# Performance work log

Measured on AMD Instinct MI355X. Metric: run time of the kernel, lower is better.

## Reference

```python
import jax, jax.numpy as jnp
import numpy as np

N = 8192
IN_F = 512
OUT_F = 64
ALPHA = 0.2        # LeakyReLU slope
L_ITERS = 3        # RobustSum iterations
EPS = 0.01
GAMMA = 4.0
T = 1.0
NEG_BIG = -9e15


def setup_inputs() -> dict:
    key = jax.random.key(0)
    k1, k2, k3, k4 = jax.random.split(key, 4)
    x = jax.random.normal(k1, (N, IN_F), dtype=jnp.float32)
    adj = jax.random.randint(k2, (N, N), 0, 2, dtype=jnp.int32)
    # xavier-uniform-like init scales
    limW = 1.414 * np.sqrt(6.0 / (IN_F + OUT_F))
    W = jax.random.uniform(k3, (IN_F, OUT_F), dtype=jnp.float32, minval=-limW, maxval=limW)
    lima = 1.414 * np.sqrt(6.0 / (2 * OUT_F + 1))
    a = jax.random.uniform(k4, (2 * OUT_F, 1), dtype=jnp.float32, minval=-lima, maxval=lima)
    return {"adj": adj, "input": x, "W": W, "a": a}


def _robust_sum_mcp(A, V):
    # M = A @ V, then IRLS-style reweighted aggregation (norm='MCP')
    M = A @ V
    for _ in range(L_ITERS):
        Md = jax.lax.stop_gradient(M)
        Vd = jax.lax.stop_gradient(V)
        # pairwise Euclidean distance [N, N] (fused form of torch.cdist)
        d2 = (jnp.sum(Md * Md, axis=1, keepdims=True)
              + jnp.sum(Vd * Vd, axis=1)[None, :]
              - 2.0 * (Md @ Vd.T))
        dist = jnp.sqrt(jnp.maximum(d2, 0.0))
        w = 1.0 / (dist + EPS) - 1.0 / GAMMA
        w = jnp.maximum(w, EPS)          # w[w < eps] = eps
        ww = w * A
        denom = jnp.maximum(jnp.sum(jnp.abs(ww), axis=-1, keepdims=True), 1e-12)
        ww_norm = ww / denom             # F.normalize(p=1, dim=-1)
        M = (1.0 - T) * M + T * (ww_norm @ V)
    return M


def reference(adj, input, W, a):
    adj_f = adj.astype(jnp.float32)
    h = input @ W                                     # [N, OUT_F]
    a1 = a[:OUT_F, 0]                                 # [OUT_F]
    a2 = a[OUT_F:, 0]                                 # [OUT_F]
    # fused equivalent of cat([h_i, h_j]) @ a : e_ij = lrelu(h_i.a1 + h_j.a2)
    e = jax.nn.leaky_relu((h @ a1)[:, None] + (h @ a2)[None, :], ALPHA)  # [N, N]
    scores = adj_f * e + (1.0 - adj_f) * NEG_BIG
    attention = jax.nn.softmax(scores, axis=1)
    # dropout omitted (eval mode / dropout=0.0)
    h_prime = _robust_sum_mcp(attention, h)
    return jax.nn.elu(h_prime)                        # concat=True
```

## Files before the change

kernel.cpp:

```cpp
#include <hip/hip_runtime.h>
#include <hip/hip_bf16.h>

typedef __attribute__((ext_vector_type(8))) short s8v;
typedef __attribute__((ext_vector_type(4))) short s4v;
typedef __attribute__((ext_vector_type(4))) float f4v;

static __device__ __forceinline__ short f2bf(float f){
  unsigned int u = __float_as_uint(f);
  u = (u + 0x7FFFu + ((u >> 16) & 1u)) >> 16;
  return (short)u;
}

static __device__ __forceinline__ s4v pack4(float a, float b, float c, float d){
  union { s4v v; __hip_bfloat162 h[2]; } u;
  u.h[0] = __float22bfloat162_rn(make_float2(a, b));
  u.h[1] = __float22bfloat162_rn(make_float2(c, d));
  return u.v;
}

static __device__ __forceinline__ f4v mfma16(s4v a, s4v b, f4v c){
  return __builtin_amdgcn_mfma_f32_16x16x16bf16_1k(a, b, c, 0, 0, 0);
}

__global__ __launch_bounds__(256) void k_h(const float* __restrict__ x,
                                           const float* __restrict__ W,
                                           float* __restrict__ h){
  int wid = threadIdx.x >> 6, lane = threadIdx.x & 63;
  int r0 = (blockIdx.x * 4 + wid) * 8;
  const float* xr = x + (size_t)r0 * 512;
  float acc[8] = {0.f,0.f,0.f,0.f,0.f,0.f,0.f,0.f};
  #pragma unroll 4
  for (int k = 0; k < 512; ++k){
    float wv = W[k*64 + lane];
    #pragma unroll
    for (int r = 0; r < 8; ++r)
      acc[r] = fmaf(xr[(size_t)r*512 + k], wv, acc[r]);
  }
  #pragma unroll
  for (int r = 0; r < 8; ++r)
    h[(size_t)(r0 + r)*64 + lane] = acc[r];
}

__global__ __launch_bounds__(256) void k_prep(const float* __restrict__ h,
                                              const float* __restrict__ a,
                                              short* __restrict__ VbfSw,
                                              short* __restrict__ VTsw,
                                              float* __restrict__ F,
                                              float2* __restrict__ EG,
                                              float* __restrict__ V2arr,
                                              float* __restrict__ Pv2,
                                              float* __restrict__ Pv2x,
                                              float* __restrict__ Pg,
                                              float* __restrict__ Vpart){
  __shared__ float t[64][65];
  const int tid = threadIdx.x;
  const int lane = tid & 63, w = tid >> 6;
  const int lo = lane & 15, hi = lane >> 4;
  const int i0 = blockIdx.x * 64;
  #pragma unroll
  for (int it = 0; it < 16; ++it){
    int r = w * 16 + it;
    t[r][lane] = h[(size_t)(i0 + r) * 64 + lane];
  }
  __syncthreads();
  #pragma unroll
  for (int ks = 0; ks < 2; ++ks){
    s8v o;
    #pragma unroll
    for (int e = 0; e < 8; ++e)
      o[e] = f2bf(t[w*16 + lo][ks*32 + hi*8 + e]);
    *(s8v*)(VbfSw + ((size_t)(i0/16 + w)*2 + ks)*512 + lane*8) = o;
  }
  const int p = w >> 1;
  #pragma unroll
  for (int oo = 0; oo < 2; ++oo){
    const int ot = (w & 1) * 2 + oo;
    s8v o;
    #pragma unroll
    for (int e = 0; e < 8; ++e){
      int parity = e >> 2, q = e & 3;
      o[e] = f2bf(t[(p*2 + parity)*16 + hi*4 + q][ot*16 + lo]);
    }
    *(s8v*)(VTsw + ((size_t)(i0/32 + p)*4 + ot)*512 + lane*8) = o;
  }
  if (tid < 64){
    const int r = tid;
    float f = 0.f, g = 0.f, v2 = 0.f;
    #pragma unroll 8
    for (int o = 0; o < 64; ++o){
      float hv = t[r][o];
      f  = fmaf(hv, a[o],      f);
      g  = fmaf(hv, a[64 + o], g);
      v2 = fmaf(hv, hv,        v2);
    }
    const int row = i0 + r;
    F[row] = f;
    V2arr[row] = v2;
    EG[row] = make_float2(__expf(g), __expf(0.2f * g));
    float vmin = v2, vmax = v2, gmx = g;
    #pragma unroll
    for (int off = 32; off; off >>= 1){
      vmin = fminf(vmin, __shfl_xor(vmin, off));
      vmax = fmaxf(vmax, __shfl_xor(vmax, off));
      gmx  = fmaxf(gmx,  __shfl_xor(gmx,  off));
    }
    if (r == 0){ Pv2[blockIdx.x] = vmin; Pv2x[blockIdx.x] = vmax; Pg[blockIdx.x] = gmx; }
    float cs = 0.f;
    #pragma unroll 8
    for (int rr = 0; rr < 64; ++rr) cs += t[rr][tid];
    Vpart[(size_t)blockIdx.x * 64 + tid] = cs;
  }
}

__global__ __launch_bounds__(512, 4) void k_fused(
    const int* __restrict__ adj,
    const float2* __restrict__ EG, const float* __restrict__ V2arr,
    const float* __restrict__ F,
    const float* __restrict__ Pv2, const float* __restrict__ Pv2x,
    const float* __restrict__ Pg,
    const float* __restrict__ Vpart,
    const short* __restrict__ VbfSw, const short* __restrict__ VTsw,
    unsigned long long* __restrict__ adjbits,
    float* __restrict__ out)
{
  __shared__ float numT[8][64][16];
  __shared__ float denL[8][16];
  __shared__ float Mlds[16][68];
  __shared__ float M1L[16][68];
  __shared__ __align__(16) short Mb16[16][64];
  __shared__ float CiL[16], rm2L[16], uaiL[16];
  __shared__ float VmeanL[64];
  __shared__ float TminS[128], TmaxS[128];
  __shared__ float gmaxS, v2minS, rmnS, rmxS;
  __shared__ int actL, chgL, emptyL;

  const int tid  = threadIdx.x;
  const int w    = tid >> 6;
  const int lane = tid & 63;
  const int lo = lane & 15, hi = lane >> 4;
  const int r0 = blockIdx.x << 4;
  const int i  = r0 + lo;

  if (tid < 64){
    float v = fminf(Pv2[tid], Pv2[tid + 64]);
    float g = fmaxf(Pg[tid],  Pg[tid + 64]);
    #pragma unroll
    for (int off = 32; off; off >>= 1){
      v = fminf(v, __shfl_xor(v, off));
      g = fmaxf(g, __shfl_xor(g, off));
    }
    if (tid == 0){ v2minS = v; gmaxS = g; actL = 0; emptyL = 0; }
  }
  if (tid >= 64 && tid < 192){
    const int b = tid - 64;
    TminS[b] = sqrtf(Pv2[b]);
    TmaxS[b] = sqrtf(Pv2x[b]);
  }
  __syncthreads();

  const float fi   = F[i];
  const float gmax = gmaxS;
  const float z    = fi + gmax;
  const float B    = fmaxf(z, 0.2f * z);
  const float e1s  = __expf(fi - B);
  const float e2s  = __expf(0.2f * fi - B);

  const int* arow = adj + (size_t)i * 8192 + hi*4;

  const f4v zero4 = {0.f,0.f,0.f,0.f};
  f4v pacc[4] = {zero4, zero4, zero4, zero4};
  float pden = 0.f;

  for (int c = w; c < 128; c += 8){
    const int* ap = arow + (c << 6);
    s4v wwpk[4];
    unsigned long long mrow = 0ull;
    #pragma unroll
    for (int nt = 0; nt < 4; ++nt){
      const int jb = (c << 6) + nt*16 + hi*4;
      const int4 av4 = *(const int4*)(ap + nt*16);
      const int ab[4] = {av4.x, av4.y, av4.z, av4.w};
      const f4v u0 = *(const f4v*)(EG + jb);
      const f4v u1 = *(const f4v*)(EG + jb + 2);
      const float ega[4] = {u0[0], u0[2], u1[0], u1[2]};
      const float egb[4] = {u0[1], u0[3], u1[1], u1[3]};
      float wwv[4];
      #pragma unroll
      for (int q = 0; q < 4; ++q){
        float u = fmaxf(e1s * ega[q], e2s * egb[q]);
        u = ab[q] ? u : 0.f;
        pden += u;
        wwv[q] = u;
      }
      const unsigned nib = (unsigned)ab[0] | ((unsigned)ab[1] << 1)
                         | ((unsigned)ab[2] << 2) | ((unsigned)ab[3] << 3);
      mrow |= (unsigned long long)nib << (nt*16 + hi*4);
      wwpk[nt] = pack4(wwv[0], wwv[1], wwv[2], wwv[3]);
    }
    mrow |= __shfl_xor(mrow, 16);
    mrow |= __shfl_xor(mrow, 32);
    if (hi == 0) adjbits[(size_t)c * 8192 + i] = mrow;

    const short* vt = VTsw + (size_t)c*4096 + lane*8;
    #pragma unroll
    for (int p = 0; p < 2; ++p){
      #pragma unroll
      for (int ot = 0; ot < 4; ++ot){
        s8v v8 = *(const s8v*)(vt + (p*4 + ot)*512);
        s4v aLo = {v8[0], v8[1], v8[2], v8[3]};
        s4v aHi = {v8[4], v8[5], v8[6], v8[7]};
        pacc[ot] = mfma16(aLo, wwpk[2*p],   pacc[ot]);
        pacc[ot] = mfma16(aHi, wwpk[2*p+1], pacc[ot]);
      }
    }
  }

  pden += __shfl_xor(pden, 16);
  pden += __shfl_xor(pden, 32);
  if (lane < 16) denL[w][lane] = pden;
  #pragma unroll
  for (int ot = 0; ot < 4; ++ot)
    #pragma unroll
    for (int q = 0; q < 4; ++q)
      numT[w][ot*16 + hi*4 + q][lo] = pacc[ot][q];
  __syncthreads();

  {
    const int ii = tid & 15;
    const int o  = tid >> 4;
    float den = 0.f;
    #pragma unroll
    for (int w2 = 0; w2 < 8; ++w2) den += denL[w2][ii];
    if (o == 0){
      uaiL[ii] = (den <= 0.f) ? (1.0f / 8192.0f) : 0.f;
      if (den <= 0.f) emptyL = 1;
    }
    den = fmaxf(den, 1e-30f);
    const float rden = 1.0f / den;
    #pragma unroll
    for (int rep = 0; rep < 2; ++rep){
      const int oo = o + rep*32;
      float num = 0.f;
      #pragma unroll
      for (int w2 = 0; w2 < 8; ++w2) num += numT[w2][oo][ii];
      Mlds[ii][oo] = num * rden;
    }
    if (tid < 16){
      float fb = F[r0 + tid];
      float zb = fb + gmax;
      float Bb = fmaxf(zb, 0.2f * zb);
      CiL[tid] = Bb + __logf(den);
    }
  }
  __syncthreads();

  if (emptyL){
    if (tid < 64){
      float s = 0.f;
      for (int b = 0; b < 128; ++b) s += Vpart[(size_t)b*64 + tid];
      VmeanL[tid] = s * (1.0f / 8192.0f);
    }
    __syncthreads();
    {
      const int r = tid >> 5, c2 = (tid & 31) << 1;
      if (uaiL[r] > 0.f){ Mlds[r][c2] = VmeanL[c2]; Mlds[r][c2+1] = VmeanL[c2+1]; }
    }
    __syncthreads();
  }

  if (tid < 16){
    float s2 = 0.f;
    #pragma unroll 8
    for (int o = 0; o < 64; ++o) s2 = fmaf(Mlds[tid][o], Mlds[tid][o], s2);
    rm2L[tid] = s2;
    if (sqrtf(s2) > sqrtf(v2minS) - 3.85f) actL = 1;
    float mn = s2, mx = s2;
    #pragma unroll
    for (int off = 8; off; off >>= 1){
      mn = fminf(mn, __shfl_xor(mn, off));
      mx = fmaxf(mx, __shfl_xor(mx, off));
    }
    if (tid == 0){ rmnS = sqrtf(mn); rmxS = sqrtf(mx); }
  }
  __syncthreads();

  if (actL){
    {
      const int r = tid >> 5, c2 = (tid & 31) << 1;
      float a0 = Mlds[r][c2], a1 = Mlds[r][c2+1];
      M1L[r][c2] = a0;  M1L[r][c2+1] = a1;
      Mb16[r][c2] = f2bf(a0); Mb16[r][c2+1] = f2bf(a1);
    }
    const float e1c = __expf(fi - CiL[lo]);
    const float e2c = __expf(0.2f * fi - CiL[lo]);
    const float uai = uaiL[lo];
    __syncthreads();

    for (int pass = 0; pass < 3; ++pass){
      if (tid == 0) chgL = 0;
      __syncthreads();
      const float rm2 = rm2L[lo];
      const float gHi = rmxS + 4.35f;
      const float gLo = rmnS - 4.35f;
      s8v bM[2];
      #pragma unroll
      for (int ks = 0; ks < 2; ++ks)
        bM[ks] = *(const s8v*)&Mb16[lo][ks*32 + hi*8];

      f4v cacc[4] = {zero4, zero4, zero4, zero4};
      float cden = 0.f;

      for (int c = w; c < 128; c += 8){
        if (TminS[c] > gHi || TmaxS[c] < gLo) continue;
        f4v acc[4] = {zero4, zero4, zero4, zero4};
        const short* vb = VbfSw + (size_t)c*4096 + lane*8;
        #pragma unroll
        for (int nt = 0; nt < 4; ++nt){
          #pragma unroll
          for (int ks = 0; ks < 2; ++ks){
            s8v av = *(const s8v*)(vb + (nt*2 + ks)*512);
            acc[nt] = __builtin_amdgcn_mfma_f32_16x16x32_bf16(av, bM[ks], acc[nt], 0, 0, 0);
          }
        }
        f4v d2s[4];
        float dmin = 1e30f;
        #pragma unroll
        for (int nt = 0; nt < 4; ++nt){
          const int jb = (c << 6) + nt*16 + hi*4;
          const f4v v2q = *(const f4v*)(V2arr + jb);
          #pragma unroll
          for (int q = 0; q < 4; ++q){
            float d2 = fmaf(-2.0f, acc[nt][q], rm2 + v2q[q]);
            d2s[nt][q] = d2;
            dmin = fminf(dmin, d2);
          }
        }
        if (__any(dmin < 14.75f)){
          const unsigned long long mrow = adjbits[(size_t)c * 8192 + i];
          s4v wwpk[4];
          #pragma unroll
          for (int nt = 0; nt < 4; ++nt){
            const int jb = (c << 6) + nt*16 + hi*4;
            const unsigned nib = (unsigned)(mrow >> (nt*16 + hi*4)) & 0xFu;
            const f4v u0 = *(const f4v*)(EG + jb);
            const f4v u1 = *(const f4v*)(EG + jb + 2);
            const float ega[4] = {u0[0], u0[2], u1[0], u1[2]};
            const float egb[4] = {u0[1], u0[3], u1[1], u1[3]};
            float wwv[4];
            #pragma unroll
            for (int q = 0; q < 4; ++q){
              float A = fmaxf(e1c * ega[q], e2c * egb[q]);
              A = ((nib >> q) & 1u) ? A : uai;
              float dist  = sqrtf(fmaxf(d2s[nt][q], 0.f));
              float delta = fmaxf(__builtin_amdgcn_rcpf(dist + 0.01f) - 0.26f, 0.f);
              float ww = delta * A;
              cden += ww;
              wwv[q] = ww;
            }
            wwpk[nt] = pack4(wwv[0], wwv[1], wwv[2], wwv[3]);
          }
          const short* vt = VTsw + (size_t)c*4096 + lane*8;
          #pragma unroll
          for (int p = 0; p < 2; ++p){
            #pragma unroll
            for (int ot = 0; ot < 4; ++ot){
              s8v v8 = *(const s8v*)(vt + (p*4 + ot)*512);
              s4v aLo = {v8[0], v8[1], v8[2], v8[3]};
              s4v aHi = {v8[4], v8[5], v8[6], v8[7]};
              cacc[ot] = mfma16(aLo, wwpk[2*p],   cacc[ot]);
              cacc[ot] = mfma16(aHi, wwpk[2*p+1], cacc[ot]);
            }
          }
        }
      }

      if (__any(cden > 0.f)) chgL = 1;
      __syncthreads();
      if (!chgL) break;
      {
        float cd = cden;
        cd += __shfl_xor(cd, 16);
        cd += __shfl_xor(cd, 32);
        if (lane < 16) denL[w][lane] = cd;
        #pragma unroll
        for (int ot = 0; ot < 4; ++ot)
          #pragma unroll
          for (int q = 0; q < 4; ++q)
            numT[w][ot*16 + hi*4 + q][lo] = cacc[ot][q];
        __syncthreads();
        {
          const int ii = tid & 15;
          const int o  = tid >> 4;
          float den = 0.f;
          #pragma unroll
          for (int w2 = 0; w2 < 8; ++w2) den += denL[w2][ii];
          const float rden = 1.0f / (0.01f + den);
          #pragma unroll
          for (int rep = 0; rep < 2; ++rep){
            const int oo = o + rep*32;
            float num = 0.f;
            #pragma unroll
            for (int w2 = 0; w2 < 8; ++w2) num += numT[w2][oo][ii];
            Mlds[ii][oo] = fmaf(0.01f, M1L[ii][oo], num) * rden;
          }
        }
        __syncthreads();
        {
          const int r = tid >> 5, c2 = (tid & 31) << 1;
          Mb16[r][c2]   = f2bf(Mlds[r][c2]);
          Mb16[r][c2+1] = f2bf(Mlds[r][c2+1]);
        }
        if (tid < 16){
          float s2 = 0.f;
          #pragma unroll 8
          for (int o = 0; o < 64; ++o) s2 = fmaf(Mlds[tid][o], Mlds[tid][o], s2);
          rm2L[tid] = s2;
          float mn = s2, mx = s2;
          #pragma unroll
          for (int off = 8; off; off >>= 1){
            mn = fminf(mn, __shfl_xor(mn, off));
            mx = fmaxf(mx, __shfl_xor(mx, off));
          }
          if (tid == 0){ rmnS = sqrtf(mn); rmxS = sqrtf(mx); }
        }
        __syncthreads();
      }
    }
  }
  __syncthreads();

  #pragma unroll
  for (int rr = 0; rr < 2; ++rr){
    const int ir = w*2 + rr;
    const float v = Mlds[ir][lane];
    out[(size_t)(r0 + ir) * 64 + lane] = (v > 0.f) ? v : (__expf(v) - 1.0f);
  }
}

extern "C" void kernel_launch(void* const* d_in, const int* in_sizes, int n_in,
                              void* d_out, int out_size, void* d_ws, size_t ws_size,
                              hipStream_t stream){
  (void)in_sizes; (void)n_in; (void)out_size; (void)ws_size;
  const int*   adj = (const int*)d_in[0];
  const float* x   = (const float*)d_in[1];
  const float* W   = (const float*)d_in[2];
  const float* a   = (const float*)d_in[3];
  float* out = (float*)d_out;
  char* ws = (char*)d_ws;

  float* h     = (float*)(ws);
  short* VbfSw = (short*)(ws + (2u << 20));
  short* VTsw  = (short*)(ws + (3u << 20));
  float* F     = (float*)(ws + (4u << 20));
  float* V2arr = (float*)(ws + (4u << 20) + (32u << 10));
  float2* EG   = (float2*)(ws + (4u << 20) + (64u << 10));
  float* Vpart = (float*)(ws + (4u << 20) + (128u << 10));
  float* Pv2   = (float*)(ws + (4u << 20) + (160u << 10));
  float* Pg    = (float*)(ws + (4u << 20) + (161u << 10));
  float* Pv2x  = (float*)(ws + (4u << 20) + (162u << 10));
  unsigned long long* adjbits = (unsigned long long*)(ws + (5u << 20));

  k_h    <<<256, 256, 0, stream>>>(x, W, h);
  k_prep <<<128, 256, 0, stream>>>(h, a, VbfSw, VTsw, F, EG, V2arr, Pv2, Pv2x, Pg, Vpart);
  k_fused<<<512, 512, 0, stream>>>(adj, EG, V2arr, F, Pv2, Pv2x, Pg, Vpart, VbfSw, VTsw, adjbits, out);
}
```

Measured before the change: 142.8 us.

## Skip stale far column tiles in IRLS passes, prefetch adj, retile input projection

Three changes. The input projection kernel now handles 4 rows per wave instead of 8, reads x as float4 and launches twice as many blocks. The first adjacency sweep prefetches the next chunk's adjacency ints into registers while working on the current chunk. In the reweighting passes, each wave records the minimum row-to-column distance per tile and, across passes, adds a bound on how far the M rows have moved; a tile is skipped when that stale minimum still exceeds the cutoff. This saves distance-MFMA work in later passes at the cost of extra reductions, shared-memory atomics and a barrier per pass, and it relies on the distance bound being conservative enough to keep results correct.

```diff
diff --git a/kernel.cpp b/kernel.cpp
--- a/kernel.cpp
+++ b/kernel.cpp
@@ -26,18 +26,23 @@
                                            const float* __restrict__ W,
                                            float* __restrict__ h){
   int wid = threadIdx.x >> 6, lane = threadIdx.x & 63;
-  int r0 = (blockIdx.x * 4 + wid) * 8;
+  int r0 = (blockIdx.x * 4 + wid) * 4;
   const float* xr = x + (size_t)r0 * 512;
-  float acc[8] = {0.f,0.f,0.f,0.f,0.f,0.f,0.f,0.f};
-  #pragma unroll 4
-  for (int k = 0; k < 512; ++k){
-    float wv = W[k*64 + lane];
-    #pragma unroll
-    for (int r = 0; r < 8; ++r)
-      acc[r] = fmaf(xr[(size_t)r*512 + k], wv, acc[r]);
+  float acc[4] = {0.f,0.f,0.f,0.f};
+  #pragma unroll 2
+  for (int k = 0; k < 512; k += 4){
+    const float w0 = W[(k+0)*64 + lane];
+    const float w1 = W[(k+1)*64 + lane];
+    const float w2 = W[(k+2)*64 + lane];
+    const float w3 = W[(k+3)*64 + lane];
+    #pragma unroll
+    for (int r = 0; r < 4; ++r){
+      const float4 xv = *(const float4*)(xr + (size_t)r*512 + k);
+      acc[r] = fmaf(xv.x, w0, fmaf(xv.y, w1, fmaf(xv.z, w2, fmaf(xv.w, w3, acc[r]))));
+    }
   }
   #pragma unroll
-  for (int r = 0; r < 8; ++r)
+  for (int r = 0; r < 4; ++r)
     h[(size_t)(r0 + r)*64 + lane] = acc[r];
 }
 
@@ -131,6 +136,9 @@
   __shared__ float CiL[16], rm2L[16], uaiL[16];
   __shared__ float VmeanL[64];
   __shared__ float TminS[128], TmaxS[128];
+  __shared__ float aminS[8][16], staleS[8][16];
+  __shared__ float d2rowS[16];
+  __shared__ float dMaxS;
   __shared__ float gmaxS, v2minS, rmnS, rmxS;
   __shared__ int actL, chgL, emptyL;
 
@@ -171,15 +179,26 @@
   f4v pacc[4] = {zero4, zero4, zero4, zero4};
   float pden = 0.f;
 
+  int4 curA[4];
+  {
+    const int* ap0 = arow + (w << 6);
+    #pragma unroll
+    for (int nt = 0; nt < 4; ++nt) curA[nt] = *(const int4*)(ap0 + nt*16);
+  }
   for (int c = w; c < 128; c += 8){
-    const int* ap = arow + (c << 6);
+    const int cn = c + 8;
+    int4 nxtA[4];
+    if (cn < 128){
+      const int* ap2 = arow + (cn << 6);
+      #pragma unroll
+      for (int nt = 0; nt < 4; ++nt) nxtA[nt] = *(const int4*)(ap2 + nt*16);
+    }
     s4v wwpk[4];
     unsigned long long mrow = 0ull;
     #pragma unroll
     for (int nt = 0; nt < 4; ++nt){
       const int jb = (c << 6) + nt*16 + hi*4;
-      const int4 av4 = *(const int4*)(ap + nt*16);
-      const int ab[4] = {av4.x, av4.y, av4.z, av4.w};
+      const int ab[4] = {curA[nt].x, curA[nt].y, curA[nt].z, curA[nt].w};
       const f4v u0 = *(const f4v*)(EG + jb);
       const f4v u1 = *(const f4v*)(EG + jb + 2);
       const float ega[4] = {u0[0], u0[2], u1[0], u1[2]};
@@ -213,6 +232,10 @@
         pacc[ot] = mfma16(aHi, wwpk[2*p+1], pacc[ot]);
       }
     }
+    if (cn < 128){
+      #pragma unroll
+      for (int nt = 0; nt < 4; ++nt) curA[nt] = nxtA[nt];
+    }
   }
 
   pden += __shfl_xor(pden, 16);
@@ -291,6 +314,8 @@
       M1L[r][c2] = a0;  M1L[r][c2+1] = a1;
       Mb16[r][c2] = f2bf(a0); Mb16[r][c2+1] = f2bf(a1);
     }
+    if (tid < 128){ aminS[tid >> 4][tid & 15] = 0.f; staleS[tid >> 4][tid & 15] = 0.f; }
+    if (tid < 16) d2rowS[tid] = 0.f;
     const float e1c = __expf(fi - CiL[lo]);
     const float e2c = __expf(0.2f * fi - CiL[lo]);
     const float uai = uaiL[lo];
@@ -311,6 +336,8 @@
       float cden = 0.f;
 
       for (int c = w; c < 128; c += 8){
+        const int t = (c - w) >> 3;
+        if (aminS[w][t] > 4.0f + staleS[w][t]) continue;
         if (TminS[c] > gHi || TmaxS[c] < gLo) continue;
         f4v acc[4] = {zero4, zero4, zero4, zero4};
         const short* vb = VbfSw + (size_t)c*4096 + lane*8;
@@ -335,6 +362,10 @@
             dmin = fminf(dmin, d2);
           }
         }
+        float dm = dmin;
+        #pragma unroll
+        for (int off = 32; off; off >>= 1) dm = fminf(dm, __shfl_xor(dm, off));
+        if (lane == 0){ aminS[w][t] = sqrtf(fmaxf(dm, 0.f)); staleS[w][t] = 0.f; }
         if (__any(dmin < 14.75f)){
           const unsigned long long mrow = adjbits[(size_t)c * 8192 + i];
           s4v wwpk[4];
@@ -395,14 +426,22 @@
           #pragma unroll
           for (int w2 = 0; w2 < 8; ++w2) den += denL[w2][ii];
           const float rden = 1.0f / (0.01f + den);
+          float dsum = 0.f;
           #pragma unroll
           for (int rep = 0; rep < 2; ++rep){
             const int oo = o + rep*32;
             float num = 0.f;
             #pragma unroll
             for (int w2 = 0; w2 < 8; ++w2) num += numT[w2][oo][ii];
-            Mlds[ii][oo] = fmaf(0.01f, M1L[ii][oo], num) * rden;
+            const float nv = fmaf(0.01f, M1L[ii][oo], num) * rden;
+            const float od = Mlds[ii][oo];
+            const float df = nv - od;
+            dsum = fmaf(df, df, dsum);
+            Mlds[ii][oo] = nv;
           }
+          dsum += __shfl_xor(dsum, 16);
+          dsum += __shfl_xor(dsum, 32);
+          if (lane < 16) atomicAdd(&d2rowS[lane], dsum);
         }
         __syncthreads();
         {
@@ -422,7 +461,14 @@
             mx = fmaxf(mx, __shfl_xor(mx, off));
           }
           if (tid == 0){ rmnS = sqrtf(mn); rmxS = sqrtf(mx); }
+          float dm2 = d2rowS[tid];
+          #pragma unroll
+          for (int off = 8; off; off >>= 1) dm2 = fmaxf(dm2, __shfl_xor(dm2, off));
+          if (tid == 0) dMaxS = sqrtf(dm2) + 0.15f;
         }
+        __syncthreads();
+        if (tid < 128) staleS[tid >> 4][tid & 15] += dMaxS;
+        if (tid < 16) d2rowS[tid] = 0.f;
         __syncthreads();
       }
     }
@@ -460,7 +506,7 @@
   float* Pv2x  = (float*)(ws + (4u << 20) + (162u << 10));
   unsigned long long* adjbits = (unsigned long long*)(ws + (5u << 20));
 
-  k_h    <<<256, 256, 0, stream>>>(x, W, h);
+  k_h    <<<512, 256, 0, stream>>>(x, W, h);
   k_prep <<<128, 256, 0, stream>>>(h, a, VbfSw, VTsw, F, EG, V2arr, Pv2, Pv2x, Pg, Vpart);
   k_fused<<<512, 512, 0, stream>>>(adj, EG, V2arr, F, Pv2, Pv2x, Pg, Vpart, VbfSw, VTsw, adjbits, out);
 }
```

New measurement: 147.1 us. 3.0% more time.
